# Kernel optimization log

Hardware: AMD Instinct MI355X
Metric: run time of the kernel (lower is better)

## Reference

```python
import jax, jax.numpy as jnp
import numpy as np

# ---- db4 filters (pywt conventions: dec_lo = rec_lo[::-1], rec_hi = qmf(rec_lo)) ----
F = 8  # db4 filter length
_rec_lo = np.array([0.23037781330885523, 0.7148465705525415, 0.6308807679295904,
                    -0.027983769416983849, -0.18703481171888114, 0.030841381835986965,
                    0.032883011666982945, -0.010597401784997278], dtype=np.float32)
_rec_hi = _rec_lo[::-1].copy()
_rec_hi[1::2] *= -1.0
REC_LO = jnp.asarray(_rec_lo)
REC_HI = jnp.asarray(_rec_hi)

MAX_LEVEL = 9  # pywt.dwt_max_level(4096, 8)


def _conv1d(x, kernel, stride=1, padding='VALID', lhs_dilation=None):
    # x: [B, L] -> correlation (XLA conv does NOT flip the kernel)
    out = jax.lax.conv_general_dilated(
        x[:, None, :], kernel[None, None, :],
        window_strides=(stride,), padding=padding,
        lhs_dilation=lhs_dilation,
        dimension_numbers=('NCH', 'OIH', 'NCH'))
    return out[:, 0, :]


def dwt(x):
    # pywt.dwt(x, 'db4', mode='symmetric'):
    # cA = np.convolve(sym_ext(x, F-1), dec_lo, 'valid')[1::2]
    # convolution with dec filter == correlation with rec filter (its reverse)
    ext = jnp.pad(x, ((0, 0), (F - 1, F - 1)), mode='symmetric')[:, 1:]
    return _conv1d(ext, REC_LO, stride=2), _conv1d(ext, REC_HI, stride=2)


def idwt(ca, cd):
    # pywt.idwt: zero-upsample coeffs, full convolution with rec filters, trim edges
    n = ca.shape[1]
    pad = ((F - 1, F - 1),)
    out = (_conv1d(ca, REC_LO[::-1], padding=pad, lhs_dilation=(2,)) +
           _conv1d(cd, REC_HI[::-1], padding=pad, lhs_dilation=(2,)))
    return out[:, F - 2:2 * n]  # output length = 2n - F + 2


def wavelet_features(x1):
    # Faithful to WaveletDWTLayer stack + WaveletParsingLayer: at each level k>=2,
    # reconstruct with details of levels k and k-1 only (others zeroed), with
    # pywt.waverec's trim-by-one rule; concatenate the 8 full-length reconstructions.
    a = x1
    cds, recs = [], []
    for level in range(1, MAX_LEVEL + 1):
        a, d = dwt(a)
        if level >= 2:
            r = idwt(jnp.zeros_like(d), d)
            for j in range(level - 2, -1, -1):
                dj = cds[j] if j == level - 2 else jnp.zeros_like(cds[j])
                if r.shape[1] == dj.shape[1] + 1:  # waverec trim rule
                    r = r[:, :-1]
                r = idwt(r, dj)
            recs.append(r)  # [B, signal_length]
        cds.append(d)
    return jnp.concatenate(recs, axis=1)  # [B, signal_length*(MAX_LEVEL-1)]


def reference(x1, x2, x3, W0, b0, W1, b1, W2, b2):
    # x2/x3 are placeholders in the original module (overwritten by layers 1/2)
    h = wavelet_features(x1)
    for W, b in ((W0, b0), (W1, b1), (W2, b2)):
        h = jax.nn.relu(h) @ W.T + b
    return h


def setup_inputs() -> dict:
    key = jax.random.key(0)
    ks = jax.random.split(key, 4)
    B, N = 2048, 4096
    D_IN, H1, H2, OUT = 32768, 181, 13, 10
    return {
        'x1': jax.random.normal(ks[0], (B, N), jnp.float32),
        'x2': jnp.zeros((B, 1, 8), jnp.float32),
        'x3': jnp.zeros((B, 1, 8), jnp.float32),
        'W0': jax.random.normal(ks[1], (H1, D_IN), jnp.float32) / np.float32(np.sqrt(D_IN)),
        'b0': jnp.zeros((H1,), jnp.float32),
        'W1': jax.random.normal(ks[2], (H2, H1), jnp.float32) / np.float32(np.sqrt(H1)),
        'b1': jnp.zeros((H2,), jnp.float32),
        'W2': jax.random.normal(ks[3], (OUT, H2), jnp.float32) / np.float32(np.sqrt(H2)),
        'b2': jnp.zeros((OUT,), jnp.float32),
    }
```

## Files before the change

### kernel.cpp

```cpp
#include <hip/hip_runtime.h>
#include <hip/hip_bf16.h>


typedef _Float16 f16x8 __attribute__((ext_vector_type(8)));
typedef _Float16 f16x4v __attribute__((ext_vector_type(4)));
typedef float f32x4 __attribute__((ext_vector_type(4)));

#define WV_THREADS 256
#define DROW 4160
#define NSPLIT 32
#define KCHUNK 1024

#define L0 0.23037781330885523f
#define L1 0.7148465705525415f
#define L2f 0.6308807679295904f
#define L3 -0.02798376941698385f
#define L4 -0.18703481171888114f
#define L5 0.030841381835986965f
#define L6 0.032883011666982945f
#define L7 -0.010597401784997278f

#define H0 -0.010597401784997278f
#define H1 -0.032883011666982945f
#define H2 0.030841381835986965f
#define H3 0.18703481171888114f
#define H4 -0.02798376941698385f
#define H5 -0.6308807679295904f
#define H6 0.7148465705525415f
#define H7 -0.23037781330885523f

__constant__ constexpr int cNL[10]   = {4096, 2051, 1029, 518, 262, 134, 70, 38, 22, 14};
__constant__ constexpr int cDOFF[10] = {0, 0, 2052, 3084, 3604, 3868, 4004, 4076, 4116, 4140};

__device__ __forceinline__ int ext_idx(int j, int n) {
  return (j < 6) ? (5 - j) : ((j < n + 6) ? (j - 6) : (2 * n + 5 - j));
}

__device__ __forceinline__ void dwt2(const float* a, float* anext, float* d,
                                     int n, int m, bool store_a) {
  const int ng = (m + 1) >> 1;
  for (int g = threadIdx.x; g < ng; g += WV_THREADS) {
    float w[10];
    if (g >= 2 && 4 * g + 9 <= n + 5) {
      const float2* af = (const float2*)a + (2 * g - 3);
      float2 b0 = af[0], b1 = af[1], b2 = af[2], b3 = af[3], b4 = af[4];
      w[0] = b0.x; w[1] = b0.y; w[2] = b1.x; w[3] = b1.y; w[4] = b2.x;
      w[5] = b2.y; w[6] = b3.x; w[7] = b3.y; w[8] = b4.x; w[9] = b4.y;
    } else {
#pragma unroll
      for (int q = 0; q < 10; ++q) {
        int j = 4 * g + q;
        int jm = n + 12;
        if (j > jm) j = jm;
        w[q] = a[ext_idx(j, n)];
      }
    }
    float sl0 = w[0]*L0 + w[1]*L1 + w[2]*L2f + w[3]*L3 + w[4]*L4 + w[5]*L5 + w[6]*L6 + w[7]*L7;
    float sh0 = w[0]*H0 + w[1]*H1 + w[2]*H2  + w[3]*H3 + w[4]*H4 + w[5]*H5 + w[6]*H6 + w[7]*H7;
    float sl1 = w[2]*L0 + w[3]*L1 + w[4]*L2f + w[5]*L3 + w[6]*L4 + w[7]*L5 + w[8]*L6 + w[9]*L7;
    float sh1 = w[2]*H0 + w[3]*H1 + w[4]*H2  + w[5]*H3 + w[6]*H4 + w[7]*H5 + w[8]*H6 + w[9]*H7;
    if (2 * g + 1 < m) {
      if (store_a) *(float2*)(anext + 2 * g) = make_float2(sl0, sl1);
      *(float2*)(d + 2 * g) = make_float2(sh0, sh1);
    } else {
      if (store_a) anext[2 * g] = sl0;
      d[2 * g] = sh0;
    }
  }
}

#define SWZ(u) ((u) ^ (((u) >> 3) & 7))
__device__ __forceinline__ const float4* lds4c(const float* b, int s) {
  return (const float4*)b + SWZ(s);
}
__device__ __forceinline__ float4* lds4(float* b, int s) {
  return (float4*)b + SWZ(s);
}

template <bool HAS_CA, bool HAS_CD, bool FINAL, int N>
__device__ __forceinline__ void step16(const float* ca, const float* cd,
                                       float* outl, _Float16* outg) {
  constexpr int npair = N - 3;
  constexpr int ng = (npair + 7) >> 3;
  const int t = threadIdx.x;
  if (t >= ng) return;
  float w[12], v[12];
  if constexpr (HAS_CA) {
    float4 a = *lds4c(ca, 2 * t), b = *lds4c(ca, 2 * t + 1), c = *lds4c(ca, 2 * t + 2);
    w[0]=a.x; w[1]=a.y; w[2]=a.z; w[3]=a.w; w[4]=b.x; w[5]=b.y; w[6]=b.z; w[7]=b.w;
    w[8]=c.x; w[9]=c.y; w[10]=c.z; w[11]=c.w;
  }
  if constexpr (HAS_CD) {
    const float4* p = (const float4*)(cd + 8 * t);
    float4 a = p[0], b = p[1], c = p[2];
    v[0]=a.x; v[1]=a.y; v[2]=a.z; v[3]=a.w; v[4]=b.x; v[5]=b.y; v[6]=b.z; v[7]=b.w;
    v[8]=c.x; v[9]=c.y; v[10]=c.z; v[11]=c.w;
  }
  float E[8], O[8];
#pragma unroll
  for (int pp = 0; pp < 8; ++pp) {
    float e = 0.f, o = 0.f;
    if constexpr (HAS_CA) {
      e = w[pp+3]*L0 + w[pp+2]*L2f + w[pp+1]*L4 + w[pp]*L6;
      o = w[pp+3]*L1 + w[pp+2]*L3  + w[pp+1]*L5 + w[pp]*L7;
    }
    if constexpr (HAS_CD) {
      e += v[pp+3]*H0 + v[pp+2]*H2 + v[pp+1]*H4 + v[pp]*H6;
      o += v[pp+3]*H1 + v[pp+2]*H3 + v[pp+1]*H5 + v[pp]*H7;
    }
    E[pp] = e; O[pp] = o;
  }
  if constexpr (FINAL) {
    f16x8 h0, h1;
    h0[0]=(_Float16)fmaxf(E[0],0.f); h0[1]=(_Float16)fmaxf(O[0],0.f);
    h0[2]=(_Float16)fmaxf(E[1],0.f); h0[3]=(_Float16)fmaxf(O[1],0.f);
    h0[4]=(_Float16)fmaxf(E[2],0.f); h0[5]=(_Float16)fmaxf(O[2],0.f);
    h0[6]=(_Float16)fmaxf(E[3],0.f); h0[7]=(_Float16)fmaxf(O[3],0.f);
    h1[0]=(_Float16)fmaxf(E[4],0.f); h1[1]=(_Float16)fmaxf(O[4],0.f);
    h1[2]=(_Float16)fmaxf(E[5],0.f); h1[3]=(_Float16)fmaxf(O[5],0.f);
    h1[4]=(_Float16)fmaxf(E[6],0.f); h1[5]=(_Float16)fmaxf(O[6],0.f);
    h1[6]=(_Float16)fmaxf(E[7],0.f); h1[7]=(_Float16)fmaxf(O[7],0.f);
    *(f16x8*)(outg + 16 * t) = h0;
    *(f16x8*)(outg + 16 * t + 8) = h1;
  } else {
#pragma unroll
    for (int j = 0; j < 4; ++j) {
      const int p2 = 8 * t + 2 * j;
      if (p2 + 1 < npair) {
        *lds4(outl, 4 * t + j) = make_float4(E[2*j], O[2*j], E[2*j+1], O[2*j+1]);
      } else if (p2 < npair) {
        *(float2*)lds4(outl, 4 * t + j) = make_float2(E[2*j], O[2*j]);
      }
    }
  }
}

__device__ __forceinline__ void nocd2_core(const float w[12], float r[11],
                                           float E[8], float O[8]) {
#pragma unroll
  for (int h = 0; h < 6; ++h) {
    float e = w[h+3]*L0 + w[h+2]*L2f + w[h+1]*L4 + w[h]*L6;
    float o = w[h+3]*L1 + w[h+2]*L3  + w[h+1]*L5 + w[h]*L7;
    r[2*h] = e;
    if (2*h + 1 < 11) r[2*h+1] = o;
  }
#pragma unroll
  for (int pp = 0; pp < 8; ++pp) {
    E[pp] = r[pp+3]*L0 + r[pp+2]*L2f + r[pp+1]*L4 + r[pp]*L6;
    O[pp] = r[pp+3]*L1 + r[pp+2]*L3  + r[pp+1]*L5 + r[pp]*L7;
  }
}

template <int N1>
__device__ __forceinline__ void pair16(const float* cur, float* outl) {
  constexpr int N2 = (2 * N1 - 6 == 1030) ? 1029 : (2 * N1 - 6);
  constexpr int np2 = N2 - 3;
  constexpr int ng = (np2 + 7) >> 3;
  const int t = threadIdx.x;
  if (t >= ng) return;
  float w[12];
  float4 a = *lds4c(cur, t), b = *lds4c(cur, t + 1), c = *lds4c(cur, t + 2);
  w[0]=a.x; w[1]=a.y; w[2]=a.z; w[3]=a.w; w[4]=b.x; w[5]=b.y; w[6]=b.z; w[7]=b.w;
  w[8]=c.x; w[9]=c.y; w[10]=c.z; w[11]=c.w;
  float r[11], E[8], O[8];
  nocd2_core(w, r, E, O);
#pragma unroll
  for (int j = 0; j < 4; ++j) {
    const int p2 = 8 * t + 2 * j;
    if (p2 + 1 < np2) {
      *lds4(outl, 4 * t + j) = make_float4(E[2*j], O[2*j], E[2*j+1], O[2*j+1]);
    } else if (p2 < np2) {
      *(float2*)lds4(outl, 4 * t + j) = make_float2(E[2*j], O[2*j]);
    }
  }
}

__device__ __forceinline__ void finpair16(const float* cur, _Float16* outg) {
  const int t = threadIdx.x;
  float w[12];
  float4 a = *lds4c(cur, t), b = *lds4c(cur, t + 1), c = *lds4c(cur, t + 2);
  w[0]=a.x; w[1]=a.y; w[2]=a.z; w[3]=a.w; w[4]=b.x; w[5]=b.y; w[6]=b.z; w[7]=b.w;
  w[8]=c.x; w[9]=c.y; w[10]=c.z; w[11]=c.w;
  float r[11], E[8], O[8];
  nocd2_core(w, r, E, O);
  f16x8 h0, h1;
  h0[0]=(_Float16)fmaxf(E[0],0.f); h0[1]=(_Float16)fmaxf(O[0],0.f);
  h0[2]=(_Float16)fmaxf(E[1],0.f); h0[3]=(_Float16)fmaxf(O[1],0.f);
  h0[4]=(_Float16)fmaxf(E[2],0.f); h0[5]=(_Float16)fmaxf(O[2],0.f);
  h0[6]=(_Float16)fmaxf(E[3],0.f); h0[7]=(_Float16)fmaxf(O[3],0.f);
  h1[0]=(_Float16)fmaxf(E[4],0.f); h1[1]=(_Float16)fmaxf(O[4],0.f);
  h1[2]=(_Float16)fmaxf(E[5],0.f); h1[3]=(_Float16)fmaxf(O[5],0.f);
  h1[4]=(_Float16)fmaxf(E[6],0.f); h1[5]=(_Float16)fmaxf(O[6],0.f);
  h1[6]=(_Float16)fmaxf(E[7],0.f); h1[7]=(_Float16)fmaxf(O[7],0.f);
  *(f16x8*)(outg + 16 * t) = h0;
  *(f16x8*)(outg + 16 * t + 8) = h1;
}

template <int NL, int NLm1>
__device__ __forceinline__ void initpair16(const float* cdL, const float* cdm,
                                           float* outl) {
  constexpr int np2 = NLm1 - 3;
  constexpr int ng = (np2 + 7) >> 3;
  const int t = threadIdx.x;
  if (t >= ng) return;
  float w[12];
  {
    const float4* p = (const float4*)(cdL + 4 * t);
    float4 a = p[0], b = p[1], c = p[2];
    w[0]=a.x; w[1]=a.y; w[2]=a.z; w[3]=a.w; w[4]=b.x; w[5]=b.y; w[6]=b.z; w[7]=b.w;
    w[8]=c.x; w[9]=c.y; w[10]=c.z; w[11]=c.w;
  }
  float r[11];
#pragma unroll
  for (int h = 0; h < 6; ++h) {
    float e = w[h+3]*H0 + w[h+2]*H2 + w[h+1]*H4 + w[h]*H6;
    float o = w[h+3]*H1 + w[h+2]*H3 + w[h+1]*H5 + w[h]*H7;
    r[2*h] = e;
    if (2*h + 1 < 11) r[2*h+1] = o;
  }
  float v[12];
  {
    const float4* p = (const float4*)(cdm + 8 * t);
    float4 a = p[0], b = p[1], c = p[2];
    v[0]=a.x; v[1]=a.y; v[2]=a.z; v[3]=a.w; v[4]=b.x; v[5]=b.y; v[6]=b.z; v[7]=b.w;
    v[8]=c.x; v[9]=c.y; v[10]=c.z; v[11]=c.w;
  }
  float E[8], O[8];
#pragma unroll
  for (int pp = 0; pp < 8; ++pp) {
    E[pp] = r[pp+3]*L0 + r[pp+2]*L2f + r[pp+1]*L4 + r[pp]*L6
          + v[pp+3]*H0 + v[pp+2]*H2  + v[pp+1]*H4 + v[pp]*H6;
    O[pp] = r[pp+3]*L1 + r[pp+2]*L3  + r[pp+1]*L5 + r[pp]*L7
          + v[pp+3]*H1 + v[pp+2]*H3  + v[pp+1]*H5 + v[pp]*H7;
  }
#pragma unroll
  for (int j = 0; j < 4; ++j) {
    const int p2 = 8 * t + 2 * j;
    if (p2 + 1 < np2) {
      *lds4(outl, 4 * t + j) = make_float4(E[2*j], O[2*j], E[2*j+1], O[2*j+1]);
    } else if (p2 < np2) {
      *(float2*)lds4(outl, 4 * t + j) = make_float2(E[2*j], O[2*j]);
    }
  }
}

template <int L>
__device__ __forceinline__ void synth2(const float* dr, _Float16* og,
                                       float* s1, float* s2) {
  if constexpr (L == 2) {
    step16<false, true, false, 1029>(nullptr, dr + cDOFF[2], s1, nullptr);
    __syncthreads();
    step16<true, true, true, 2051>(s1, dr + cDOFF[1], nullptr, og);
  } else {
    initpair16<cNL[L], cNL[L - 1]>(dr + cDOFF[L], dr + cDOFF[L - 1], s1);
    __syncthreads();
    if constexpr (L == 3) {
      step16<true, false, true, 2051>(s1, nullptr, nullptr, og);
    } else if constexpr (L == 4) {
      finpair16(s1, og);
    } else if constexpr (L == 5) {
      pair16<518>(s1, s2); __syncthreads();
      step16<true, false, true, 2051>(s2, nullptr, nullptr, og);
    } else if constexpr (L == 6) {
      pair16<262>(s1, s2); __syncthreads();
      finpair16(s2, og);
    } else if constexpr (L == 7) {
      pair16<134>(s1, s2); __syncthreads();
      pair16<518>(s2, s1); __syncthreads();
      step16<true, false, true, 2051>(s1, nullptr, nullptr, og);
    } else if constexpr (L == 8) {
      pair16<70>(s1, s2); __syncthreads();
      pair16<262>(s2, s1); __syncthreads();
      finpair16(s1, og);
    } else {
      pair16<38>(s1, s2); __syncthreads();
      pair16<134>(s1 ? s2 : s2, s1); __syncthreads();
      pair16<518>(s1, s2); __syncthreads();
      step16<true, false, true, 2051>(s2, nullptr, nullptr, og);
    }
  }
}

__global__ __launch_bounds__(WV_THREADS) void wv_analysis_cvt(
    const float* __restrict__ x, float* __restrict__ dG,
    const float* __restrict__ W0, _Float16* __restrict__ Bw) {
  __shared__ float r1[4104];
  __shared__ float r2[2056];
  const int tid = threadIdx.x;

  if (blockIdx.x >= 2048) {
    size_t i = ((size_t)(blockIdx.x - 2048) * 256 + tid) * 4;
    int rowc = (int)(i >> 15);
    f16x4v h;
    if (rowc < 181) {
      const float4 v = *(const float4*)(W0 + i);
      h[0] = (_Float16)v.x; h[1] = (_Float16)v.y;
      h[2] = (_Float16)v.z; h[3] = (_Float16)v.w;
    } else {
      h[0] = (_Float16)0.f; h[1] = (_Float16)0.f;
      h[2] = (_Float16)0.f; h[3] = (_Float16)0.f;
    }
    *(f16x4v*)(Bw + i) = h;
    return;
  }

  const int NLa[10]  = {4096, 2051, 1029, 518, 262, 134, 70, 38, 22, 14};
  const int DOFF[10] = {0, 0, 2052, 3084, 3604, 3868, 4004, 4076, 4116, 4140};
  const int LOFF[10] = {0, 0, 1036, 520, 2068, 1040, 2332, 1176, 2404, 1216};
  const int row = blockIdx.x;

  const float4* xr = (const float4*)(x + (size_t)row * 4096);
  for (int i = tid; i < 1024; i += WV_THREADS) ((float4*)r1)[i] = xr[i];
  __syncthreads();

  float* dr = dG + (size_t)row * DROW;
  dwt2(r1, r2, dr + DOFF[1], NLa[0], NLa[1], true);
  __syncthreads();
  const float* ap = r2;
  float* an = r1;
  for (int lev = 2; lev <= 9; ++lev) {
    float* dbuf = ((lev & 1) ? r2 : r1) + LOFF[lev];
    dwt2(ap, an, dbuf, NLa[lev - 1], NLa[lev], lev < 9);
    __syncthreads();
    const float* t = ap; ap = an; an = (float*)t;
  }
  for (int lev = 2; lev <= 9; ++lev) {
    const float* src = ((lev & 1) ? r2 : r1) + LOFF[lev];
    float* dst = dr + DOFF[lev];
    const int n = NLa[lev];
    for (int i = 2 * tid; i + 1 < n; i += 2 * WV_THREADS)
      *(float2*)(dst + i) = *(const float2*)(src + i);
    if ((n & 1) && tid == 0) dst[n - 1] = src[n - 1];
  }
}

__global__ __launch_bounds__(WV_THREADS, 8) void wv_synth(
    const float* __restrict__ dG, _Float16* __restrict__ A) {
  __shared__ alignas(16) float s1[2080];
  __shared__ alignas(16) float s2[2080];
  const int row = blockIdx.x;
  const float* dr = dG + (size_t)row * DROW;
  _Float16* og = A + (size_t)row * 32768 + (size_t)blockIdx.y * 4096;
  switch (blockIdx.y) {
    case 0: synth2<2>(dr, og, s1, s2); break;
    case 1: synth2<3>(dr, og, s1, s2); break;
    case 2: synth2<4>(dr, og, s1, s2); break;
    case 3: synth2<5>(dr, og, s1, s2); break;
    case 4: synth2<6>(dr, og, s1, s2); break;
    case 5: synth2<7>(dr, og, s1, s2); break;
    case 6: synth2<8>(dr, og, s1, s2); break;
    default: synth2<9>(dr, og, s1, s2); break;
  }
}

__device__ __forceinline__ void load_lds16(const void* g, void* l) {
  __builtin_amdgcn_global_load_lds((__attribute__((address_space(1))) unsigned int*)g,
                                   (__attribute__((address_space(3))) unsigned int*)l,
                                   16, 0, 0);
}

__global__ __launch_bounds__(256, 2) void gemm_kernel(
    const _Float16* __restrict__ A, const _Float16* __restrict__ Bw,
    float* __restrict__ P) {
  __shared__ _Float16 As[128 * 64];
  __shared__ _Float16 Bs[192 * 64];
  const int tid = threadIdx.x;
  const int lane = tid & 63;
  const int wave = tid >> 6;
  const int m0 = blockIdx.x * 128;
  const int k_idx = blockIdx.y;
  const int k0 = k_idx * KCHUNK;

  f32x4 acc[2][12];
#pragma unroll
  for (int mt = 0; mt < 2; ++mt)
#pragma unroll
    for (int nt = 0; nt < 12; ++nt) acc[mt][nt] = (f32x4){0.f, 0.f, 0.f, 0.f};

  for (int ks = 0; ks < (KCHUNK >> 6); ++ks) {
    const int kbase = k0 + (ks << 6);
    __syncthreads();
#pragma unroll
    for (int t = 0; t < 4; ++t) {
      int g = ((wave * 4 + t) << 6) + lane;
      int r = g >> 3, cs = g & 7;
      const _Float16* gp = A + (size_t)(m0 + r) * 32768 + kbase + ((cs ^ (r & 7)) << 3);
      load_lds16(gp, (char*)As + (size_t)((wave * 4 + t) << 10));
    }
#pragma unroll
    for (int t = 0; t < 6; ++t) {
      int g = ((wave * 6 + t) << 6) + lane;
      int r = g >> 3, cs = g & 7;
      const _Float16* gp = Bw + (size_t)r * 32768 + kbase + ((cs ^ (r & 7)) << 3);
      load_lds16(gp, (char*)Bs + (size_t)((wave * 6 + t) << 10));
    }
    __syncthreads();
#pragma unroll
    for (int kk = 0; kk < 2; ++kk) {
      const int chunk = kk * 4 + (lane >> 4);
      f16x8 af[2];
#pragma unroll
      for (int mt = 0; mt < 2; ++mt) {
        int r = wave * 32 + mt * 16 + (lane & 15);
        af[mt] = *(const f16x8*)(As + r * 64 + ((chunk ^ (r & 7)) << 3));
      }
#pragma unroll
      for (int nt = 0; nt < 12; ++nt) {
        int rb = nt * 16 + (lane & 15);
        f16x8 bf = *(const f16x8*)(Bs + rb * 64 + ((chunk ^ (rb & 7)) << 3));
        acc[0][nt] = __builtin_amdgcn_mfma_f32_16x16x32_f16(af[0], bf, acc[0][nt], 0, 0, 0);
        acc[1][nt] = __builtin_amdgcn_mfma_f32_16x16x32_f16(af[1], bf, acc[1][nt], 0, 0, 0);
      }
    }
  }
  float* Pp = P + ((size_t)k_idx * 2048 + m0) * 192;
#pragma unroll
  for (int mt = 0; mt < 2; ++mt)
#pragma unroll
    for (int nt = 0; nt < 12; ++nt)
#pragma unroll
      for (int r4 = 0; r4 < 4; ++r4) {
        int rr = wave * 32 + mt * 16 + ((lane >> 4) << 2) + r4;
        int cc = nt * 16 + (lane & 15);
        Pp[(size_t)rr * 192 + cc] = acc[mt][nt][r4];
      }
}

__global__ __launch_bounds__(256) void mlp_kernel(
    const float* __restrict__ P, const float* __restrict__ b0,
    const float* __restrict__ W1, const float* __restrict__ b1,
    const float* __restrict__ W2, const float* __restrict__ b2,
    float* __restrict__ out) {
  __shared__ float part[4][193];
  __shared__ float h1[192];
  __shared__ float h2[13];
  const int row = blockIdx.x;
  const int t = threadIdx.x;
  const int g = t >> 6;
  const int l = t & 63;

  float a0 = 0.f, a1 = 0.f, a2 = 0.f;
  for (int si = 0; si < NSPLIT / 4; ++si) {
    int s = g + (si << 2);
    const float* Pr = P + ((size_t)s * 2048 + row) * 192;
    a0 += Pr[l]; a1 += Pr[64 + l]; a2 += Pr[128 + l];
  }
  part[g][l] = a0; part[g][64 + l] = a1; part[g][128 + l] = a2;
  __syncthreads();

  if (t < 192) {
    float v = part[0][t] + part[1][t] + part[2][t] + part[3][t];
    h1[t] = (t < 181) ? fmaxf(v + b0[t], 0.f) : 0.f;
  }
  __syncthreads();

#pragma unroll
  for (int r = 0; r < 4; ++r) {
    int j = g + (r << 2);
    if (j < 13) {
      float v = 0.f;
#pragma unroll
      for (int q = 0; q < 3; ++q) {
        int n = l + (q << 6);
        if (n < 181) v += h1[n] * W1[j * 181 + n];
      }
      for (int off = 32; off >= 1; off >>= 1) v += __shfl_down(v, off);
      if (l == 0) h2[j] = fmaxf(v + b1[j], 0.f);
    }
  }
  __syncthreads();

  if (t < 10) {
    float c = b2[t];
#pragma unroll
    for (int j = 0; j < 13; ++j) c += h2[j] * W2[t * 13 + j];
    out[(size_t)row * 10 + t] = c;
  }
}

extern "C" void kernel_launch(void* const* d_in, const int* in_sizes, int n_in,
                              void* d_out, int out_size, void* d_ws, size_t ws_size,
                              hipStream_t stream) {
  const float* x1 = (const float*)d_in[0];
  const float* W0 = (const float*)d_in[3];
  const float* b0 = (const float*)d_in[4];
  const float* W1 = (const float*)d_in[5];
  const float* b1 = (const float*)d_in[6];
  const float* W2 = (const float*)d_in[7];
  const float* b2 = (const float*)d_in[8];
  float* out = (float*)d_out;

  char* ws = (char*)d_ws;
  const size_t A_BYTES = (size_t)2048 * 32768 * 2;
  const size_t B_BYTES = (size_t)192 * 32768 * 2;
  _Float16* Afeat = (_Float16*)ws;
  _Float16* Bw = (_Float16*)(ws + A_BYTES);
  float* Dq = (float*)(ws + A_BYTES + B_BYTES);
  float* P = (float*)(ws + A_BYTES + B_BYTES);

  wv_analysis_cvt<<<2048 + 6144, WV_THREADS, 0, stream>>>(x1, Dq, W0, Bw);
  dim3 sg(2048, 8);
  wv_synth<<<sg, WV_THREADS, 0, stream>>>(Dq, Afeat);
  dim3 gg(16, NSPLIT);
  gemm_kernel<<<gg, 256, 0, stream>>>(Afeat, Bw, P);
  mlp_kernel<<<2048, 256, 0, stream>>>(P, b0, W1, b1, W2, b2, out);
}
```

Before: 223.0 us.

## Double-buffer GEMM LDS tiles and widen M tile to 256 rows

The fp16 feature GEMM now uses 512 threads per block and a 256-row M tile. Its LDS stages are double-buffered, so the global-to-LDS loads for the next K step are issued while MFMAs run on the current buffer. This removes one barrier per K step and is meant to hide load latency behind compute. In exchange, LDS use rises to about 112KB per block and the grid halves, which lowers occupancy and the number of blocks in flight. A redundant ternary in the level-9 synthesis path is also simplified.

```diff
diff --git a/kernel.cpp b/kernel.cpp
--- a/kernel.cpp
+++ b/kernel.cpp
@@ -10,6 +10,7 @@
 #define DROW 4160
 #define NSPLIT 32
 #define KCHUNK 1024
+#define GEMM_BM 256
 
 #define L0 0.23037781330885523f
 #define L1 0.7148465705525415f
@@ -274,7 +275,7 @@
       finpair16(s1, og);
     } else {
       pair16<38>(s1, s2); __syncthreads();
-      pair16<134>(s1 ? s2 : s2, s1); __syncthreads();
+      pair16<134>(s2, s1); __syncthreads();
       pair16<518>(s1, s2); __syncthreads();
       step16<true, false, true, 2051>(s2, nullptr, nullptr, og);
     }
@@ -359,15 +360,15 @@
                                    16, 0, 0);
 }
 
-__global__ __launch_bounds__(256, 2) void gemm_kernel(
+__global__ __launch_bounds__(512, 2) void gemm_kernel(
     const _Float16* __restrict__ A, const _Float16* __restrict__ Bw,
     float* __restrict__ P) {
-  __shared__ _Float16 As[128 * 64];
-  __shared__ _Float16 Bs[192 * 64];
+  __shared__ _Float16 As[2][GEMM_BM * 64];
+  __shared__ _Float16 Bs[2][192 * 64];
   const int tid = threadIdx.x;
   const int lane = tid & 63;
   const int wave = tid >> 6;
-  const int m0 = blockIdx.x * 128;
+  const int m0 = blockIdx.x * GEMM_BM;
   const int k_idx = blockIdx.y;
   const int k0 = k_idx * KCHUNK;
 
@@ -377,24 +378,32 @@
 #pragma unroll
     for (int nt = 0; nt < 12; ++nt) acc[mt][nt] = (f32x4){0.f, 0.f, 0.f, 0.f};
 
-  for (int ks = 0; ks < (KCHUNK >> 6); ++ks) {
+  auto stage = [&](int ks, int b) {
     const int kbase = k0 + (ks << 6);
-    __syncthreads();
 #pragma unroll
     for (int t = 0; t < 4; ++t) {
-      int g = ((wave * 4 + t) << 6) + lane;
+      int c = wave * 4 + t;
+      int g = (c << 6) + lane;
       int r = g >> 3, cs = g & 7;
       const _Float16* gp = A + (size_t)(m0 + r) * 32768 + kbase + ((cs ^ (r & 7)) << 3);
-      load_lds16(gp, (char*)As + (size_t)((wave * 4 + t) << 10));
-    }
-#pragma unroll
-    for (int t = 0; t < 6; ++t) {
-      int g = ((wave * 6 + t) << 6) + lane;
+      load_lds16(gp, (char*)As[b] + ((size_t)c << 10));
+    }
+#pragma unroll
+    for (int t = 0; t < 3; ++t) {
+      int c = wave * 3 + t;
+      int g = (c << 6) + lane;
       int r = g >> 3, cs = g & 7;
       const _Float16* gp = Bw + (size_t)r * 32768 + kbase + ((cs ^ (r & 7)) << 3);
-      load_lds16(gp, (char*)Bs + (size_t)((wave * 6 + t) << 10));
-    }
-    __syncthreads();
+      load_lds16(gp, (char*)Bs[b] + ((size_t)c << 10));
+    }
+  };
+
+  stage(0, 0);
+  __syncthreads();
+
+  for (int ks = 0; ks < (KCHUNK >> 6); ++ks) {
+    const int cur = ks & 1;
+    if (ks + 1 < (KCHUNK >> 6)) stage(ks + 1, cur ^ 1);
 #pragma unroll
     for (int kk = 0; kk < 2; ++kk) {
       const int chunk = kk * 4 + (lane >> 4);
@@ -402,17 +411,19 @@
 #pragma unroll
       for (int mt = 0; mt < 2; ++mt) {
         int r = wave * 32 + mt * 16 + (lane & 15);
-        af[mt] = *(const f16x8*)(As + r * 64 + ((chunk ^ (r & 7)) << 3));
+        af[mt] = *(const f16x8*)(As[cur] + r * 64 + ((chunk ^ (r & 7)) << 3));
       }
 #pragma unroll
       for (int nt = 0; nt < 12; ++nt) {
         int rb = nt * 16 + (lane & 15);
-        f16x8 bf = *(const f16x8*)(Bs + rb * 64 + ((chunk ^ (rb & 7)) << 3));
+        f16x8 bf = *(const f16x8*)(Bs[cur] + rb * 64 + ((chunk ^ (rb & 7)) << 3));
         acc[0][nt] = __builtin_amdgcn_mfma_f32_16x16x32_f16(af[0], bf, acc[0][nt], 0, 0, 0);
         acc[1][nt] = __builtin_amdgcn_mfma_f32_16x16x32_f16(af[1], bf, acc[1][nt], 0, 0, 0);
       }
     }
-  }
+    __syncthreads();
+  }
+
   float* Pp = P + ((size_t)k_idx * 2048 + m0) * 192;
 #pragma unroll
   for (int mt = 0; mt < 2; ++mt)
@@ -501,7 +512,7 @@
   wv_analysis_cvt<<<2048 + 6144, WV_THREADS, 0, stream>>>(x1, Dq, W0, Bw);
   dim3 sg(2048, 8);
   wv_synth<<<sg, WV_THREADS, 0, stream>>>(Dq, Afeat);
-  dim3 gg(16, NSPLIT);
-  gemm_kernel<<<gg, 256, 0, stream>>>(Afeat, Bw, P);
+  dim3 gg(2048 / GEMM_BM, NSPLIT);
+  gemm_kernel<<<gg, 512, 0, stream>>>(Afeat, Bw, P);
   mlp_kernel<<<2048, 256, 0, stream>>>(P, b0, W1, b1, W2, b2, out);
 }
```

Measured after the change: 224.0 us. About the same (+0.5%).
